# Performance work log

Hardware: AMD Instinct MI355X
Metric: run time of the kernel (lower is better)

Reference implementation:

```python
import jax, jax.numpy as jnp
import numpy as np

NUM_CAPS = 8
IN_CH = 768
OUT_CH = 64  # == num_routes
BATCH = 16384


def setup_inputs() -> dict:
    key = jax.random.key(0)
    ks = jax.random.split(key, 9)
    lim = 1.0 / np.sqrt(IN_CH)  # torch Linear default init range
    inp = {
        'img_emb': jax.random.normal(ks[0], (BATCH, IN_CH), jnp.float32),
        'capt_emb': jax.random.normal(ks[1], (BATCH, IN_CH), jnp.float32),
        'dct_emb': jax.random.normal(ks[2], (BATCH, IN_CH), jnp.float32),
        'W_img': jax.random.uniform(ks[3], (NUM_CAPS, OUT_CH, IN_CH), jnp.float32, -lim, lim),
        'b_img': jax.random.uniform(ks[4], (NUM_CAPS, OUT_CH), jnp.float32, -lim, lim),
        'W_capt': jax.random.uniform(ks[5], (NUM_CAPS, OUT_CH, IN_CH), jnp.float32, -lim, lim),
        'b_capt': jax.random.uniform(ks[6], (NUM_CAPS, OUT_CH), jnp.float32, -lim, lim),
        'W_dct': jax.random.uniform(ks[7], (NUM_CAPS, OUT_CH, IN_CH), jnp.float32, -lim, lim),
        'b_dct': jax.random.uniform(ks[8], (NUM_CAPS, OUT_CH), jnp.float32, -lim, lim),
    }
    return inp


def _project(x, W, b):
    # x: [B, I]; W: [C, R, I]; b: [C, R] -> [B, R, C]
    # torch: per-capsule Linear y = x @ W_c.T + b_c, viewed [B, R, 1], cat on last dim
    y = jnp.einsum('bi,cri->brc', x, W) + b.T[None]  # [B, R, C]
    return y


def _squash(u, epsilon=1e-07):
    sq = jnp.sum(u * u, axis=-1, keepdims=True)  # [B, 3R, 1]
    safe_norm = jnp.sqrt(sq + epsilon)
    return sq * u / ((1.0 + sq) * safe_norm)


def reference(img_emb, capt_emb, dct_emb, W_img, b_img, W_capt, b_capt, W_dct, b_dct):
    u_img = _project(img_emb, W_img, b_img)      # [B, 64, 8]
    u_capt = _project(capt_emb, W_capt, b_capt)  # [B, 64, 8]
    u_dct = _project(dct_emb, W_dct, b_dct)      # [B, 64, 8]
    combined = jnp.concatenate([u_img, u_capt, u_dct], axis=1)  # [B, 192, 8]
    return _squash(combined)
```

## Files before the change

kernel.cpp:

```cpp
#include <hip/hip_runtime.h>

typedef __attribute__((ext_vector_type(8))) short short8;
typedef __attribute__((ext_vector_type(4))) float floatx4;
typedef __attribute__((ext_vector_type(4))) unsigned int uintx4;

#if __has_builtin(__builtin_amdgcn_cvt_pk_bf16_f32)
typedef __attribute__((ext_vector_type(2))) __bf16 bf16x2;
__device__ __forceinline__ unsigned int pk_bf16(float a, float b) {
  bf16x2 v = __builtin_amdgcn_cvt_pk_bf16_f32(a, b);
  return __builtin_bit_cast(unsigned int, v);
}
#else
__device__ __forceinline__ unsigned int bf16_1(float f) {
  unsigned int u = __builtin_bit_cast(unsigned int, f);
  return (u + 0x7fffu + ((u >> 16) & 1u)) >> 16;
}
__device__ __forceinline__ unsigned int pk_bf16(float a, float b) {
  return bf16_1(a) | (bf16_1(b) << 16);
}
#endif


__global__ __launch_bounds__(256) void prep_w(
    const float* __restrict__ Wi, const float* __restrict__ Wc, const float* __restrict__ Wd,
    const float* __restrict__ bi, const float* __restrict__ bc, const float* __restrict__ bd,
    uintx4* __restrict__ Bprep, float* __restrict__ biasPrep) {
  const int t = blockIdx.x * 256 + threadIdx.x;
  const int l = t & 63;
  const int frag = t >> 6;
  const int nt = frag & 3;
  const int q = frag >> 2;
  const int ks = q % 24;
  const int q2 = q / 24;
  const int h = q2 & 7;
  const int mod = q2 >> 3;
  const int n16 = h * 4 + nt;
  const float* __restrict__ W = (mod == 0) ? Wi : ((mod == 1) ? Wc : Wd);

  const int n = n16 * 16 + (l & 15);
  const int r = n >> 3;
  const int c = n & 7;
  const int i0 = ks * 32 + (l >> 4) * 8;
  const float* src = W + (size_t)(c * 64 + r) * 768 + i0;
  floatx4 f0 = *(const floatx4*)(src);
  floatx4 f1 = *(const floatx4*)(src + 4);
  uintx4 p;
  p.x = pk_bf16(f0.x, f0.y);
  p.y = pk_bf16(f0.z, f0.w);
  p.z = pk_bf16(f1.x, f1.y);
  p.w = pk_bf16(f1.z, f1.w);
  Bprep[(size_t)frag * 64 + l] = p;

  if (t < 1536) {
    const int m2 = t >> 9;
    const int nn = t & 511;
    const float* bb = (m2 == 0) ? bi : ((m2 == 1) ? bc : bd);
    biasPrep[t] = bb[(nn & 7) * 64 + (nn >> 3)];
  }
}

#define STAGE(p)                                                             \
  {                                                                          \
    _Pragma("unroll") for (int i = 0; i < 6; ++i) {                          \
      const int idx = i * 4096 + tid * 4;           \
      const int m = (unsigned)idx / 384u;                                    \
      const int k = idx - m * 384;                                           \
      floatx4 f = *(const floatx4*)(srcbase + (size_t)m * 768 + (p)*384 + k);\
      const int ks = k >> 5;                         \
      const int kk = k & 31;                                                 \
      const int qk = kk >> 3;                                                \
      const int jh = (kk >> 2) & 1;                                          \
      const int mtg = m >> 4;                         \
      const int lnn = m & 15;                                                \
      const int px = (ks * 4 + qk) & 15;                \
      const int slot = (lnn ^ px) + (qk << 4);                               \
      unsigned long long w =                                                 \
          ((unsigned long long)pk_bf16(f.z, f.w) << 32) | pk_bf16(f.x, f.y); \
      As64[(((ks * 4 + mtg) * 64 + slot) << 1) + jh] = w;                    \
    }                                                                        \
  }

#define LOADA(aa, kk)                           \
  {                                                                          \
    _Pragma("unroll") for (int mt = 0; mt < 2; ++mt)                         \
        aa[mt] = Afr[((kk) * 4 + wr2 + mt) * 64 +                            \
                     ((ln ^ (((kk) * 4 + quad) & 15)) + (quad << 4))];       \
  }

#define LOADB(bb, kk)                          \
  {                                                                          \
    _Pragma("unroll") for (int n2 = 0; n2 < 4; ++n2)                         \
        bb[n2] = bbase[(size_t)((kk) * 4 + n2) * 64];                        \
  }

#define COMP(aa, bb)                                                     \
  {                                                                      \
    _Pragma("unroll") for (int mt = 0; mt < 2; ++mt)                     \
    {                                                                    \
      short8 af = __builtin_bit_cast(short8, aa[mt]);                    \
      _Pragma("unroll") for (int n2 = 0; n2 < 4; ++n2)                   \
          acc[mt][n2] = __builtin_amdgcn_mfma_f32_16x16x32_bf16(         \
              af, __builtin_bit_cast(short8, bb[n2]), acc[mt][n2], 0, 0, \
              0);                                                        \
    }                                                                    \
  }

__global__ __launch_bounds__(1024, 4) void caps_fused(
    const float* __restrict__ x0, const float* __restrict__ x1, const float* __restrict__ x2,
    const uintx4* __restrict__ Bprep, const float* __restrict__ biasPrep,
    float* __restrict__ out) {
  __shared__ unsigned long long As64[48 * 128];

  const int tid = threadIdx.x;
  const int bx0 = blockIdx.x;
  const int bx = (bx0 & 7) * 96 + (bx0 >> 3);
  const int mod = bx >> 8;
  const int bm = bx & 255;
  const float* __restrict__ X = (mod == 0) ? x0 : ((mod == 1) ? x1 : x2);
  const float* srcbase = X + (size_t)bm * 64 * 768;

  const int lane = tid & 63;
  const int ln = lane & 15;
  const int quad = lane >> 4;
  const int wv = tid >> 6;
  const int wr = wv >> 3;
  const int wc = wv & 7;
  const int wr2 = wr << 1;

  const uintx4* Afr = (const uintx4*)As64;
  const uintx4* bbase = Bprep + (size_t)(mod * 8 + wc) * (96 * 64) + lane;

  floatx4 acc[2][4] = {};
  uintx4 a0[2], a1[2], b0[4], b1[4];

  STAGE(0);
  __syncthreads();
  LOADA(a0, 0);
  LOADB(b0, 0);
#pragma unroll 1
  for (int it = 0; it < 6; ++it) {
    const int s = 2 * it;
    LOADA(a1, s + 1); LOADB(b1, s + 1);
    COMP(a0, b0);
    if (it != 5) { LOADA(a0, s + 2); LOADB(b0, s + 2); }
    COMP(a1, b1);
  }
  LOADB(b0, 12);
  __syncthreads();
  STAGE(1);
  __syncthreads();
  LOADA(a0, 0);
#pragma unroll 1
  for (int it = 0; it < 6; ++it) {
    const int s = 2 * it;
    LOADA(a1, s + 1); LOADB(b1, 12 + s + 1);
    COMP(a0, b0);
    if (it != 5) { LOADA(a0, s + 2); LOADB(b0, 12 + s + 2); }
    COMP(a1, b1);
  }

  const int col0 = mod * 512 + wc * 64 + ln;
  float bias[4];
#pragma unroll
  for (int n2 = 0; n2 < 4; ++n2) bias[n2] = biasPrep[col0 + n2 * 16];

#pragma unroll
  for (int mt = 0; mt < 2; ++mt) {
    const size_t rbase = (size_t)(bm * 64 + wr * 32 + mt * 16 + quad * 4) * 1536;
#pragma unroll
    for (int n2 = 0; n2 < 4; ++n2) {
      float* op = out + rbase + col0 + n2 * 16;
#pragma unroll
      for (int jj = 0; jj < 4; ++jj) {
        float u = acc[mt][n2][jj] + bias[n2];
        float s = u * u;
        s += __shfl_xor(s, 1);
        s += __shfl_xor(s, 2);
        s += __shfl_xor(s, 4);
#if __has_builtin(__builtin_amdgcn_rsqf) && __has_builtin(__builtin_amdgcn_rcpf)
        float sc = s * __builtin_amdgcn_rsqf(s + 1e-7f) *
                   __builtin_amdgcn_rcpf(1.0f + s);
#else
        float sc = s / ((1.0f + s) * sqrtf(s + 1e-7f));
#endif
        op[(size_t)jj * 1536] = u * sc;
      }
    }
  }
}

extern "C" void kernel_launch(void* const* d_in, const int* in_sizes, int n_in,
                              void* d_out, int out_size, void* d_ws, size_t ws_size,
                              hipStream_t stream) {
  const float* ximg = (const float*)d_in[0];
  const float* xcapt = (const float*)d_in[1];
  const float* xdct = (const float*)d_in[2];
  const float* Wi = (const float*)d_in[3];
  const float* bi = (const float*)d_in[4];
  const float* Wc = (const float*)d_in[5];
  const float* bc = (const float*)d_in[6];
  const float* Wd = (const float*)d_in[7];
  const float* bd = (const float*)d_in[8];

  uintx4* Bprep = (uintx4*)d_ws;
  float* biasPrep = (float*)((char*)d_ws + 2304 * 1024);

  hipLaunchKernelGGL(prep_w, dim3(576), dim3(256), 0, stream,
                     Wi, Wc, Wd, bi, bc, bd, Bprep, biasPrep);
  hipLaunchKernelGGL(caps_fused, dim3(768), dim3(1024), 0, stream,
                     ximg, xcapt, xdct, (const uintx4*)Bprep, biasPrep,
                     (float*)d_out);
}
```

Before: 90.50 us.

## Split capsule GEMM blocks into column halves with staggered k-order per wave

Halves the block size to 512 threads and doubles the grid so each block computes 256 of a modality's 512 output columns. Each wave also starts its k-loop at a different offset and wraps around, to spread LDS and B-fragment accesses. Smaller blocks may improve scheduling and occupancy. The cost is that every input row tile is now loaded and converted to bf16 by two blocks, doubling global input reads.

```diff
diff --git a/kernel.cpp b/kernel.cpp
--- a/kernel.cpp
+++ b/kernel.cpp
@@ -59,25 +59,25 @@
   }
 }
 
-#define STAGE(p)                                                             \
-  {                                                                          \
-    _Pragma("unroll") for (int i = 0; i < 6; ++i) {                          \
-      const int idx = i * 4096 + tid * 4;           \
-      const int m = (unsigned)idx / 384u;                                    \
-      const int k = idx - m * 384;                                           \
-      floatx4 f = *(const floatx4*)(srcbase + (size_t)m * 768 + (p)*384 + k);\
-      const int ks = k >> 5;                         \
-      const int kk = k & 31;                                                 \
-      const int qk = kk >> 3;                                                \
-      const int jh = (kk >> 2) & 1;                                          \
-      const int mtg = m >> 4;                         \
-      const int lnn = m & 15;                                                \
-      const int px = (ks * 4 + qk) & 15;                \
-      const int slot = (lnn ^ px) + (qk << 4);                               \
-      unsigned long long w =                                                 \
-          ((unsigned long long)pk_bf16(f.z, f.w) << 32) | pk_bf16(f.x, f.y); \
-      As64[(((ks * 4 + mtg) * 64 + slot) << 1) + jh] = w;                    \
-    }                                                                        \
+#define STAGE(p)                                                              \
+  {                                                                           \
+    _Pragma("unroll") for (int i = 0; i < 12; ++i) {                          \
+      const int idx = i * 2048 + tid * 4;            \
+      const int m = (unsigned)idx / 384u;                                     \
+      const int k = idx - m * 384;                                            \
+      floatx4 f = *(const floatx4*)(srcb + (size_t)m * 768 + (p) * 384 + k);  \
+      const int ks2 = k >> 5;                         \
+      const int kk = k & 31;                                                  \
+      const int qk = kk >> 3;                                                 \
+      const int jh = (kk >> 2) & 1;                                           \
+      const int mg = m >> 4;                           \
+      const int lnn = m & 15;                                                 \
+      const int px = (ks2 * 4 + qk) & 15;                \
+      const int slot = (lnn ^ px) + (qk << 4);                                \
+      unsigned long long w =                                                  \
+          ((unsigned long long)pk_bf16(f.z, f.w) << 32) | pk_bf16(f.x, f.y);  \
+      As64[(((ks2 * 4 + mg) * 64 + slot) << 1) + jh] = w;                     \
+    }                                                                         \
   }
 
 #define LOADA(aa, kk)                           \
@@ -105,7 +105,9 @@
     }                                                                    \
   }
 
-__global__ __launch_bounds__(1024, 4) void caps_fused(
+#define INCW(u) { u = (u == 11) ? 0 : (u + 1); }
+
+__global__ __launch_bounds__(512, 4) void caps_fused(
     const float* __restrict__ x0, const float* __restrict__ x1, const float* __restrict__ x2,
     const uintx4* __restrict__ Bprep, const float* __restrict__ biasPrep,
     float* __restrict__ out) {
@@ -113,67 +115,71 @@
 
   const int tid = threadIdx.x;
   const int bx0 = blockIdx.x;
-  const int bx = (bx0 & 7) * 96 + (bx0 >> 3);
-  const int mod = bx >> 8;
+  const int bx = (bx0 & 7) * 192 + (bx0 >> 3);
+  const int mod = bx >> 9;
+  const int ch = (bx >> 8) & 1;
   const int bm = bx & 255;
   const float* __restrict__ X = (mod == 0) ? x0 : ((mod == 1) ? x1 : x2);
-  const float* srcbase = X + (size_t)bm * 64 * 768;
+  const float* srcb = X + (size_t)bm * 64 * 768;
 
   const int lane = tid & 63;
   const int ln = lane & 15;
   const int quad = lane >> 4;
   const int wv = tid >> 6;
-  const int wr = wv >> 3;
-  const int wc = wv & 7;
+  const int wr = wv >> 2;
+  const int wc = wv & 3;
   const int wr2 = wr << 1;
 
   const uintx4* Afr = (const uintx4*)As64;
-  const uintx4* bbase = Bprep + (size_t)(mod * 8 + wc) * (96 * 64) + lane;
+  const uintx4* bbase =
+      Bprep + (size_t)(mod * 8 + ch * 4 + wc) * (24 * 4 * 64) + lane;
 
   floatx4 acc[2][4] = {};
   uintx4 a0[2], a1[2], b0[4], b1[4];
+  const int s0 = wc * 3;
 
   STAGE(0);
   __syncthreads();
-  LOADA(a0, 0);
-  LOADB(b0, 0);
+  int u = s0;
+  LOADA(a0, u); LOADB(b0, u); INCW(u);
 #pragma unroll 1
-  for (int it = 0; it < 6; ++it) {
-    const int s = 2 * it;
-    LOADA(a1, s + 1); LOADB(b1, s + 1);
+  for (int j = 0; j < 6; ++j) {
+    LOADA(a1, u); LOADB(b1, u); INCW(u);
     COMP(a0, b0);
-    if (it != 5) { LOADA(a0, s + 2); LOADB(b0, s + 2); }
+    if (j != 5) { LOADA(a0, u); LOADB(b0, u); INCW(u); }
     COMP(a1, b1);
   }
-  LOADB(b0, 12);
+
+  LOADB(b0, 12 + s0);
   __syncthreads();
   STAGE(1);
   __syncthreads();
-  LOADA(a0, 0);
+  u = s0;
+  LOADA(a0, u); INCW(u);
 #pragma unroll 1
-  for (int it = 0; it < 6; ++it) {
-    const int s = 2 * it;
-    LOADA(a1, s + 1); LOADB(b1, 12 + s + 1);
+  for (int j = 0; j < 6; ++j) {
+    LOADA(a1, u); LOADB(b1, 12 + u); INCW(u);
     COMP(a0, b0);
-    if (it != 5) { LOADA(a0, s + 2); LOADB(b0, 12 + s + 2); }
+    if (j != 5) { LOADA(a0, u); LOADB(b0, 12 + u); INCW(u); }
     COMP(a1, b1);
   }
 
-  const int col0 = mod * 512 + wc * 64 + ln;
+  const int col0 = mod * 512 + ch * 256 + wc * 64 + ln;
   float bias[4];
 #pragma unroll
   for (int n2 = 0; n2 < 4; ++n2) bias[n2] = biasPrep[col0 + n2 * 16];
 
 #pragma unroll
   for (int mt = 0; mt < 2; ++mt) {
-    const size_t rbase = (size_t)(bm * 64 + wr * 32 + mt * 16 + quad * 4) * 1536;
+    const size_t rbase =
+        (size_t)(bm * 64 + wr * 32 + mt * 16 + quad * 4) * 1536;
 #pragma unroll
     for (int n2 = 0; n2 < 4; ++n2) {
       float* op = out + rbase + col0 + n2 * 16;
 #pragma unroll
       for (int jj = 0; jj < 4; ++jj) {
-        float u = acc[mt][n2][jj] + bias[n2];
-        float s = u * u;
+        float uo = acc[mt][n2][jj] + bias[n2];
+        float s = uo * uo;
         s += __shfl_xor(s, 1);
         s += __shfl_xor(s, 2);
         s += __shfl_xor(s, 4);
@@ -183,7 +189,7 @@
 #else
         float sc = s / ((1.0f + s) * sqrtf(s + 1e-7f));
 #endif
-        op[(size_t)jj * 1536] = u * sc;
+        op[(size_t)jj * 1536] = uo * sc;
       }
     }
   }
@@ -207,7 +213,7 @@
 
   hipLaunchKernelGGL(prep_w, dim3(576), dim3(256), 0, stream,
                      Wi, Wc, Wd, bi, bc, bd, Bprep, biasPrep);
-  hipLaunchKernelGGL(caps_fused, dim3(768), dim3(1024), 0, stream,
+  hipLaunchKernelGGL(caps_fused, dim3(1536), dim3(512), 0, stream,
                      ximg, xcapt, xdct, (const uintx4*)Bprep, biasPrep,
                      (float*)d_out);
 }
```

New measurement: 101.3 us. 11.9% more time.
